# Performance work log

Measured on AMD Instinct MI355X. Metric: run time of the kernel, lower is better.

## Reference

```python
import jax, jax.numpy as jnp
import numpy as np

NE = 256          # number of electrons
D = 256           # attention_dim = num_heads * heads_dim
H = 4             # num_heads
DH = 64           # heads_dim
L = 2             # num_layers
NDETS = 1
MASK_LEN = 0.1


def _ln(x, s, b):
    m = jnp.mean(x, -1, keepdims=True)
    v = jnp.var(x, -1, keepdims=True)
    return (x - m) * jax.lax.rsqrt(v + 1e-5) * s + b


def setup_inputs() -> dict:
    key = jax.random.key(0)
    ks = jax.random.split(key, 16)
    n = lambda k, sh, sc: (jax.random.normal(k, sh) * sc).astype(jnp.float32)
    theta = jax.random.uniform(ks[0], (NE,), minval=0.1, maxval=np.pi - 0.1)
    phi = jax.random.uniform(ks[1], (NE,), minval=0.0, maxval=2.0 * np.pi)
    return {
        "electrons": jnp.stack([theta, phi], -1).astype(jnp.float32),
        "W_in": n(ks[2], (3, D), 3 ** -0.5),
        "Wq": n(ks[3], (L, D, H, DH), D ** -0.5),
        "bq": jnp.zeros((L, H, DH), jnp.float32),
        "Wk": n(ks[4], (L, D, H, DH), D ** -0.5),
        "bk": jnp.zeros((L, H, DH), jnp.float32),
        "Wv": n(ks[5], (L, D, H, DH), D ** -0.5),
        "bv": jnp.zeros((L, H, DH), jnp.float32),
        "Wo": n(ks[6], (L, H, DH, D), D ** -0.5),
        "bo": jnp.zeros((L, D), jnp.float32),
        "W1": n(ks[7], (L, D, D), D ** -0.5),
        "ln1_s": jnp.ones((L, D), jnp.float32),
        "ln1_b": jnp.zeros((L, D), jnp.float32),
        "W2": n(ks[8], (L, D, D), D ** -0.5),
        "b2": jnp.zeros((L, D), jnp.float32),
        "ln2_s": jnp.ones((L, D), jnp.float32),
        "ln2_b": jnp.zeros((L, D), jnp.float32),
        "Worb_r": n(ks[9], (D, NDETS * 2), D ** -0.5),
        "Worb_i": n(ks[10], (D, NDETS * 2), D ** -0.5),
    }


def reference(electrons, W_in, Wq, bq, Wk, bk, Wv, bv, Wo, bo, W1, ln1_s, ln1_b,
              W2, b2, ln2_s, ln2_b, Worb_r, Worb_i):
    theta, phi = electrons[..., 0], electrons[..., 1]
    # ---- pair gather: P = NE*(NE-1)/2 unordered pairs ----
    iu, ju = jnp.triu_indices(NE, k=1)
    th_p = jnp.stack([theta[iu], theta[ju]], -1)   # [P, 2]
    ph_p = jnp.stack([phi[iu], phi[ju]], -1)       # [P, 2]
    # input_feature: (cos t, sin t cos p, sin t sin p)
    feat = jnp.stack([jnp.cos(th_p), jnp.sin(th_p) * jnp.cos(ph_p),
                      jnp.sin(th_p) * jnp.sin(ph_p)], -1)  # [P, 2, 3]
    # ---- batched mini-transformer over all pairs (seq len 2) ----
    h = feat @ W_in  # [P, 2, D]
    for l in range(L):
        q = jnp.einsum('psd,dhk->pshk', h, Wq[l]) + bq[l]
        k = jnp.einsum('psd,dhk->pshk', h, Wk[l]) + bk[l]
        v = jnp.einsum('psd,dhk->pshk', h, Wv[l]) + bv[l]
        logits = jnp.einsum('pshk,pthk->phst', q / np.sqrt(DH), k)
        attn = jax.nn.softmax(logits, axis=-1)
        o = jnp.einsum('phst,pthk->pshk', attn, v)
        mha = jnp.einsum('pshk,hkd->psd', o, Wo[l]) + bo[l]
        h = h + mha @ W1[l]
        h = _ln(h, ln1_s[l], ln1_b[l])
        h = h + jnp.tanh(h @ W2[l] + b2[l])
        h = _ln(h, ln2_s[l], ln2_b[l])
    # ---- pair orbitals: complex dense -> [P, ndets, 2 elec, 2 orb] ----
    orb = (h @ Worb_r + 1j * (h @ Worb_i)).astype(jnp.complex64)  # [P, 2, ndets*2]
    orb = orb.reshape(-1, 2, NDETS, 2).transpose(0, 2, 1, 3)      # [P, ndets, 2, 2]
    # ---- pairwise truncation factor ----
    u = jnp.cos(th_p / 2) * jnp.exp(1j * ph_p / 2)   # [P, 2]
    v_ = jnp.sin(th_p / 2) * jnp.exp(-1j * ph_p / 2)
    chord = jnp.abs(u[:, 0] * v_[:, 1] - u[:, 1] * v_[:, 0])
    trunc = 1.0 - jnp.exp(-(chord / MASK_LEN) ** 2)  # [P]
    orb = orb * trunc[:, None, None, None]
    dets = jnp.linalg.det(orb)          # [P, ndets]
    pair_orbs = jnp.sum(dets, axis=-1)  # [P]
    # ---- scatter into antisymmetric NE x NE matrix ----
    pf = jnp.zeros((NE, NE), jnp.complex64).at[iu, ju].set(pair_orbs)
    pf = pf - pf.T
    # ---- cusp matrix ----
    ue = jnp.cos(theta / 2) * jnp.exp(0.5j * phi)   # [NE]
    ve = jnp.sin(theta / 2) * jnp.exp(-0.5j * phi)
    elem = ue[:, None] * ve[None, :] - ve[:, None] * ue[None, :]  # [NE, NE]
    eye = jnp.eye(NE, dtype=jnp.float32)
    elem_c = elem + eye
    rho_c = jnp.abs(elem_c)
    cusp = elem_c * jnp.exp(-(rho_c / MASK_LEN) ** 2)
    # ---- pfaffian = sqrt(det), in log space for stability ----
    sign, logabs = jnp.linalg.slogdet(pf + cusp)
    log_ferm = 0.5 * (logabs.astype(jnp.complex64) + 1j * jnp.angle(sign))
    # ---- bosonic flux attachment (truncated product), in log space ----
    rho = jnp.abs(elem)
    masked = jnp.sqrt(MASK_LEN ** 2 + rho ** 2) * elem / (rho + eye) + eye
    log_bos = jnp.sum(jnp.log(masked.astype(jnp.complex64)))
    return log_ferm + log_bos
```

## Files before the change

### kernel.cpp

```cpp
#include <hip/hip_runtime.h>
#include <math.h>
#include <stdint.h>

#define NE 256
#define DD 256
#define NL 2
#define P_TOT 32640
#define NB 32
#define NBP 40
#define NPANEL (NE / NB)
#define NXCD 8

typedef __bf16 bf16x8 __attribute__((ext_vector_type(8)));
typedef float f32x4 __attribute__((ext_vector_type(4)));

__device__ __forceinline__ float bf2f(ushort h) {
    union { unsigned u; float f; } c; c.u = ((unsigned)h) << 16; return c.f;
}
__device__ __forceinline__ ushort f2bf(float f) {
    union { float f; unsigned u; } c; c.f = f;
    unsigned u = c.u;
    return (ushort)((u + 0x7fffu + ((u >> 16) & 1u)) >> 16);
}

#define GLD16(gp, lp) __builtin_amdgcn_global_load_lds( \
    (const __attribute__((address_space(1))) unsigned int*)(uintptr_t)(gp), \
    (__attribute__((address_space(3))) unsigned int*)(uintptr_t)(lp), 16, 0, 0)

__global__ void idx_k(int* __restrict__ ip, int* __restrict__ jp) {
    int i = threadIdx.x;
    int base = i * 255 - (i * (i - 1)) / 2;
    for (int j = i + 1; j < NE; ++j) {
        ip[base + j - i - 1] = i;
        jp[base + j - i - 1] = j;
    }
}

__global__ void zero_k(float* __restrict__ acc) {
    if (threadIdx.x < 8) acc[threadIdx.x] = 0.f;
}

__global__ __launch_bounds__(256) void prep_w_k(
    const float* __restrict__ Wq, const float* __restrict__ Wk, const float* __restrict__ Wv,
    const float* __restrict__ Wo, const float* __restrict__ W1, const float* __restrict__ W2,
    ushort* __restrict__ Wqkv_t, ushort* __restrict__ Woth_t) {
    __shared__ float Ts[32][33];
    int z = blockIdx.z, l = z / 6, m = z % 6;
    const float* src;
    ushort* dst;
    if (m == 0)      { src = Wq + l * 65536; dst = Wqkv_t + (size_t)l * 768 * 256 + 0 * 65536; }
    else if (m == 1) { src = Wk + l * 65536; dst = Wqkv_t + (size_t)l * 768 * 256 + 1 * 65536; }
    else if (m == 2) { src = Wv + l * 65536; dst = Wqkv_t + (size_t)l * 768 * 256 + 2 * 65536; }
    else             { src = (m == 3 ? Wo : m == 4 ? W1 : W2) + l * 65536;
                       dst = Woth_t + (size_t)(l * 3 + (m - 3)) * 65536; }
    int k0 = blockIdx.x * 32, n0 = blockIdx.y * 32;
    int t = threadIdx.x, tr = t >> 5, tc = t & 31;
    for (int i = tr; i < 32; i += 8) Ts[i][tc] = src[(size_t)(k0 + i) * 256 + n0 + tc];
    __syncthreads();
    for (int i = tr; i < 32; i += 8) dst[(size_t)(n0 + i) * 256 + k0 + tc] = f2bf(Ts[tc][i]);
}

__global__ void prep_b_k(const float* __restrict__ bq, const float* __restrict__ bk,
                         const float* __restrict__ bv, float* __restrict__ bqkv) {
    int l = blockIdx.x, t = threadIdx.x;
    bqkv[l * 768 + t] = bq[l * 256 + t];
    bqkv[l * 768 + 256 + t] = bk[l * 256 + t];
    bqkv[l * 768 + 512 + t] = bv[l * 256 + t];
}

__global__ __launch_bounds__(256) void fuse_w_k(
    const float* __restrict__ Wo, const float* __restrict__ W1,
    ushort* __restrict__ Wf_t) {
    __shared__ float WoS[32][33];
    __shared__ float W1S[32][33];
    int l = blockIdx.z;
    int n0 = blockIdx.x * 32, d0 = blockIdx.y * 32;
    const float* wo = Wo + l * 65536;
    const float* w1 = W1 + l * 65536;
    int t = threadIdx.x, ty = t >> 5, tx = t & 31;
    float acc4[4] = {0.f, 0.f, 0.f, 0.f};
    for (int m0 = 0; m0 < 256; m0 += 32) {
        __syncthreads();
        for (int i = ty; i < 32; i += 8) {
            WoS[i][tx] = wo[(size_t)(d0 + i) * 256 + m0 + tx];
            W1S[i][tx] = w1[(size_t)(m0 + i) * 256 + n0 + tx];
        }
        __syncthreads();
#pragma unroll
        for (int jm = 0; jm < 32; ++jm) {
            float a = WoS[tx][jm];
#pragma unroll
            for (int q = 0; q < 4; ++q)
                acc4[q] += a * W1S[jm][ty + 8 * q];
        }
    }
#pragma unroll
    for (int q = 0; q < 4; ++q)
        Wf_t[(size_t)l * 65536 + (size_t)(n0 + ty + 8 * q) * 256 + d0 + tx] = f2bf(acc4[q]);
}

__global__ void fuse_b_k(const float* __restrict__ bo, const float* __restrict__ W1,
                         float* __restrict__ bfuse) {
    int l = blockIdx.x, n = threadIdx.x;
    const float* w1 = W1 + l * 65536;
    const float* b = bo + l * 256;
    float s = 0.f;
    for (int m = 0; m < 256; ++m) s += b[m] * w1[(size_t)m * 256 + n];
    bfuse[l * 256 + n] = s;
}

__global__ __launch_bounds__(256) void embed_k(
    const float* __restrict__ el, const float* __restrict__ Win,
    const int* __restrict__ ip, const int* __restrict__ jp,
    ushort* __restrict__ h, int P0) {
    int w = threadIdx.x >> 6, lane = threadIdx.x & 63;
    int r = blockIdx.x * 4 + w;
    int gp = P0 + (r >> 1);
    int e = (r & 1) ? jp[gp] : ip[gp];
    float th = el[2 * e], ph = el[2 * e + 1];
    float st = sinf(th);
    float f0 = cosf(th), f1 = st * cosf(ph), f2 = st * sinf(ph);
    int n = lane * 4;
    float4 w0 = *(const float4*)&Win[n];
    float4 w1 = *(const float4*)&Win[256 + n];
    float4 w2 = *(const float4*)&Win[512 + n];
    ushort4 o;
    o.x = f2bf(f0 * w0.x + f1 * w1.x + f2 * w2.x);
    o.y = f2bf(f0 * w0.y + f1 * w1.y + f2 * w2.y);
    o.z = f2bf(f0 * w0.z + f1 * w1.z + f2 * w2.z);
    o.w = f2bf(f0 * w0.w + f1 * w1.w + f2 * w2.w);
    *(ushort4*)&h[(size_t)r * 256 + n] = o;
}

template <bool BIAS, bool RES>
__global__ __launch_bounds__(256) void gemm_k(
    const ushort* __restrict__ A, int lda,
    const ushort* __restrict__ Bt,
    const float* __restrict__ bias,
    const ushort* __restrict__ Rm, int ldr,
    ushort* __restrict__ C, int ldc, int ny) {
    __shared__ ushort As[128 * 64];
    __shared__ ushort Bs[128 * 64];
    int t = threadIdx.x, lane = t & 63, w = t >> 6;
    int nwg = gridDim.x;
    int orig = blockIdx.x;
    int qq = nwg / NXCD, rr = nwg % NXCD;
    int xcd = orig % NXCD, idx = orig / NXCD;
    int wg = (xcd < rr ? xcd * (qq + 1) : rr * (qq + 1) + (xcd - rr) * qq) + idx;
    int row0 = (wg / ny) * 128, col0 = (wg % ny) * 128;
    int lrow = lane >> 3;
    int kx = ((lane & 7) ^ lrow) << 3;
    const ushort* gA = A + (size_t)(row0 + w * 32 + lrow) * lda + kx;
    const ushort* gB = Bt + (size_t)(col0 + w * 32 + lrow) * 256 + kx;
    f32x4 acc[4][4];
#pragma unroll
    for (int i = 0; i < 4; ++i)
#pragma unroll
        for (int j = 0; j < 4; ++j) acc[i][j] = (f32x4){0.f, 0.f, 0.f, 0.f};
    int wm = w >> 1, wn = w & 1;
    int mbase = wm * 64 + (lane & 15);
    int nbase = wn * 64 + (lane & 15);
    int l7 = lane & 7;
    for (int k0 = 0; k0 < 256; k0 += 64) {
        __syncthreads();
#pragma unroll
        for (int c2 = 0; c2 < 4; ++c2) {
            GLD16(gA + (size_t)(c2 * 8) * lda + k0, &As[(w * 4 + c2) * 512]);
            GLD16(gB + (size_t)(c2 * 8) * 256 + k0, &Bs[(w * 4 + c2) * 512]);
        }
        __syncthreads();
#pragma unroll
        for (int ks = 0; ks < 2; ++ks) {
            int kb = ks * 4 + (lane >> 4);
            bf16x8 af[4], bfr[4];
#pragma unroll
            for (int tm = 0; tm < 4; ++tm)
                af[tm] = *(const bf16x8*)&As[(mbase + tm * 16) * 64 + ((kb ^ l7) << 3)];
#pragma unroll
            for (int tn = 0; tn < 4; ++tn)
                bfr[tn] = *(const bf16x8*)&Bs[(nbase + tn * 16) * 64 + ((kb ^ l7) << 3)];
#pragma unroll
            for (int tm = 0; tm < 4; ++tm)
#pragma unroll
                for (int tn = 0; tn < 4; ++tn)
                    acc[tm][tn] = __builtin_amdgcn_mfma_f32_16x16x32_bf16(
                        af[tm], bfr[tn], acc[tm][tn], 0, 0, 0);
        }
    }
    int q = lane >> 4;
    int crow = row0 + wm * 64 + q * 4;
    int ccol = col0 + wn * 64 + (lane & 15);
#pragma unroll
    for (int tm = 0; tm < 4; ++tm)
#pragma unroll
        for (int r = 0; r < 4; ++r) {
            int row = crow + tm * 16 + r;
#pragma unroll
            for (int tn = 0; tn < 4; ++tn) {
                int col = ccol + tn * 16;
                float v = acc[tm][tn][r];
                if (BIAS) v += bias[col];
                if (RES) v += bf2f(Rm[(size_t)row * ldr + col]);
                C[(size_t)row * ldc + col] = f2bf(v);
            }
        }
}

__global__ __launch_bounds__(256) void attn_k(ushort* __restrict__ qkv) {
    int wid = threadIdx.x >> 6, lane = threadIdx.x & 63;
    int gw = blockIdx.x * 4 + wid;
    int p = gw >> 2, hh = gw & 3;
    size_t r0 = (size_t)(2 * p) * 768 + hh * 64 + lane;
    size_t r1 = r0 + 768;
    float q0 = bf2f(qkv[r0]) * 0.125f, q1 = bf2f(qkv[r1]) * 0.125f;
    float k0 = bf2f(qkv[r0 + 256]), k1 = bf2f(qkv[r1 + 256]);
    float v0 = bf2f(qkv[r0 + 512]), v1 = bf2f(qkv[r1 + 512]);
    float s00 = q0 * k0, s01 = q0 * k1, s10 = q1 * k0, s11 = q1 * k1;
#pragma unroll
    for (int off = 32; off; off >>= 1) {
        s00 += __shfl_xor(s00, off, 64);
        s01 += __shfl_xor(s01, off, 64);
        s10 += __shfl_xor(s10, off, 64);
        s11 += __shfl_xor(s11, off, 64);
    }
    float m0 = fmaxf(s00, s01), m1 = fmaxf(s10, s11);
    float e00 = expf(s00 - m0), e01 = expf(s01 - m0);
    float e10 = expf(s10 - m1), e11 = expf(s11 - m1);
    float i0 = 1.f / (e00 + e01), i1 = 1.f / (e10 + e11);
    float o0 = (e00 * i0) * v0 + (e01 * i0) * v1;
    float o1 = (e10 * i1) * v0 + (e11 * i1) * v1;
    qkv[r0] = f2bf(o0);
    qkv[r1] = f2bf(o1);
}

__global__ __launch_bounds__(256) void ln_a_k(
    const ushort* __restrict__ X, int ldx, ushort* __restrict__ H,
    const float* __restrict__ sc, const float* __restrict__ bi) {
    int w = threadIdx.x >> 6, lane = threadIdx.x & 63;
    int r = blockIdx.x * 4 + w;
    int d0 = lane * 4;
    ushort4 xv = *(const ushort4*)&X[(size_t)r * ldx + d0];
    float x[4] = {bf2f(xv.x), bf2f(xv.y), bf2f(xv.z), bf2f(xv.w)};
    float sum = x[0] + x[1] + x[2] + x[3];
    float sq = x[0] * x[0] + x[1] * x[1] + x[2] * x[2] + x[3] * x[3];
#pragma unroll
    for (int off = 32; off; off >>= 1) {
        sum += __shfl_xor(sum, off, 64);
        sq += __shfl_xor(sq, off, 64);
    }
    float m = sum * (1.f / 256.f);
    float var = sq * (1.f / 256.f) - m * m;
    float rs = rsqrtf(var + 1e-5f);
    float4 s4 = *(const float4*)&sc[d0];
    float4 b4 = *(const float4*)&bi[d0];
    ushort4 o;
    o.x = f2bf((x[0] - m) * rs * s4.x + b4.x);
    o.y = f2bf((x[1] - m) * rs * s4.y + b4.y);
    o.z = f2bf((x[2] - m) * rs * s4.z + b4.z);
    o.w = f2bf((x[3] - m) * rs * s4.w + b4.w);
    *(ushort4*)&H[(size_t)r * 256 + d0] = o;
}

__global__ __launch_bounds__(256) void ln_b_k(
    ushort* __restrict__ H, const ushort* __restrict__ T,
    const float* __restrict__ sc, const float* __restrict__ bi) {
    int w = threadIdx.x >> 6, lane = threadIdx.x & 63;
    int r = blockIdx.x * 4 + w;
    int d0 = lane * 4;
    ushort4 hv = *(const ushort4*)&H[(size_t)r * 256 + d0];
    ushort4 tv = *(const ushort4*)&T[(size_t)r * 256 + d0];
    float x[4];
    x[0] = bf2f(hv.x) + tanhf(bf2f(tv.x));
    x[1] = bf2f(hv.y) + tanhf(bf2f(tv.y));
    x[2] = bf2f(hv.z) + tanhf(bf2f(tv.z));
    x[3] = bf2f(hv.w) + tanhf(bf2f(tv.w));
    float sum = x[0] + x[1] + x[2] + x[3];
    float sq = x[0] * x[0] + x[1] * x[1] + x[2] * x[2] + x[3] * x[3];
#pragma unroll
    for (int off = 32; off; off >>= 1) {
        sum += __shfl_xor(sum, off, 64);
        sq += __shfl_xor(sq, off, 64);
    }
    float m = sum * (1.f / 256.f);
    float var = sq * (1.f / 256.f) - m * m;
    float rs = rsqrtf(var + 1e-5f);
    float4 s4 = *(const float4*)&sc[d0];
    float4 b4 = *(const float4*)&bi[d0];
    ushort4 o;
    o.x = f2bf((x[0] - m) * rs * s4.x + b4.x);
    o.y = f2bf((x[1] - m) * rs * s4.y + b4.y);
    o.z = f2bf((x[2] - m) * rs * s4.z + b4.z);
    o.w = f2bf((x[3] - m) * rs * s4.w + b4.w);
    *(ushort4*)&H[(size_t)r * 256 + d0] = o;
}

__global__ __launch_bounds__(256) void orb_k(
    const ushort* __restrict__ h, const float* __restrict__ Wr, const float* __restrict__ Wi,
    const float* __restrict__ el, const int* __restrict__ ip, const int* __restrict__ jp,
    float2* __restrict__ porb, int P0) {
    int w = threadIdx.x >> 6, lane = threadIdx.x & 63;
    int p = blockIdx.x * 4 + w;
    const ushort* h0 = h + (size_t)(2 * p) * 256;
    int d0 = lane * 4;
    ushort4 a0 = *(const ushort4*)&h0[d0];
    ushort4 a1 = *(const ushort4*)&h0[256 + d0];
    float x0[4] = {bf2f(a0.x), bf2f(a0.y), bf2f(a0.z), bf2f(a0.w)};
    float x1[4] = {bf2f(a1.x), bf2f(a1.y), bf2f(a1.z), bf2f(a1.w)};
    float wrv[8], wiv[8];
    *(float4*)&wrv[0] = *(const float4*)&Wr[2 * d0];
    *(float4*)&wrv[4] = *(const float4*)&Wr[2 * d0 + 4];
    *(float4*)&wiv[0] = *(const float4*)&Wi[2 * d0];
    *(float4*)&wiv[4] = *(const float4*)&Wi[2 * d0 + 4];
    float s[8] = {0, 0, 0, 0, 0, 0, 0, 0};
#pragma unroll
    for (int u = 0; u < 4; ++u) {
        s[0] += x0[u] * wrv[2 * u];     s[1] += x0[u] * wiv[2 * u];
        s[2] += x0[u] * wrv[2 * u + 1]; s[3] += x0[u] * wiv[2 * u + 1];
        s[4] += x1[u] * wrv[2 * u];     s[5] += x1[u] * wiv[2 * u];
        s[6] += x1[u] * wrv[2 * u + 1]; s[7] += x1[u] * wiv[2 * u + 1];
    }
#pragma unroll
    for (int off = 32; off; off >>= 1) {
#pragma unroll
        for (int q2 = 0; q2 < 8; ++q2) s[q2] += __shfl_xor(s[q2], off, 64);
    }
    if (lane == 0) {
        int gp = P0 + p;
        int i = ip[gp], j = jp[gp];
        float thi = el[2 * i], phi_ = el[2 * i + 1];
        float thj = el[2 * j], phj = el[2 * j + 1];
        float chi = cosf(thi * 0.5f), shi = sinf(thi * 0.5f);
        float chj = cosf(thj * 0.5f), shj = sinf(thj * 0.5f);
        float cpi = cosf(phi_ * 0.5f), spi = sinf(phi_ * 0.5f);
        float cpj = cosf(phj * 0.5f), spj = sinf(phj * 0.5f);
        float uix = chi * cpi, uiy = chi * spi;
        float vix = shi * cpi, viy = -shi * spi;
        float ujx = chj * cpj, ujy = chj * spj;
        float vjx = shj * cpj, vjy = -shj * spj;
        float crx = (uix * vjx - uiy * vjy) - (ujx * vix - ujy * viy);
        float cry = (uix * vjy + uiy * vjx) - (ujx * viy + ujy * vix);
        float chord2 = crx * crx + cry * cry;
        float trunc = 1.f - expf(-100.f * chord2);
        float t2 = trunc * trunc;
        float dr = (s[0] * s[6] - s[1] * s[7]) - (s[2] * s[4] - s[3] * s[5]);
        float di = (s[0] * s[7] + s[1] * s[6]) - (s[2] * s[5] + s[3] * s[4]);
        porb[gp] = make_float2(dr * t2, di * t2);
    }
}

__global__ __launch_bounds__(256) void assemble_k(
    const float* __restrict__ el, const float2* __restrict__ porb,
    float2* __restrict__ Am, float* acc) {
    __shared__ float sre[256], sim[256];
    int idx = blockIdx.x * 256 + threadIdx.x;
    int i = idx >> 8, j = idx & 255;
    float thi = el[2 * i], phi_ = el[2 * i + 1];
    float thj = el[2 * j], phj = el[2 * j + 1];
    float chi = cosf(thi * 0.5f), shi = sinf(thi * 0.5f);
    float chj = cosf(thj * 0.5f), shj = sinf(thj * 0.5f);
    float cpi = cosf(phi_ * 0.5f), spi = sinf(phi_ * 0.5f);
    float cpj = cosf(phj * 0.5f), spj = sinf(phj * 0.5f);
    float uix = chi * cpi, uiy = chi * spi;
    float vix = shi * cpi, viy = -shi * spi;
    float ujx = chj * cpj, ujy = chj * spj;
    float vjx = shj * cpj, vjy = -shj * spj;
    float ex = (uix * vjx - uiy * vjy) - (ujx * vix - ujy * viy);
    float ey = (uix * vjy + uiy * vjx) - (ujx * viy + ujy * vix);
    float pfx = 0.f, pfy = 0.f;
    if (i < j) {
        int pp = i * 255 - (i * (i - 1)) / 2 + (j - i - 1);
        float2 t = porb[pp]; pfx = t.x; pfy = t.y;
    } else if (i > j) {
        int pp = j * 255 - (j * (j - 1)) / 2 + (i - j - 1);
        float2 t = porb[pp]; pfx = -t.x; pfy = -t.y;
    }
    float eye = (i == j) ? 1.f : 0.f;
    float ecx = ex + eye, ecy = ey;
    float wgt = expf(-100.f * (ecx * ecx + ecy * ecy));
    Am[idx] = make_float2(pfx + ecx * wgt, pfy + ecy * wgt);
    float lre = 0.f, lim = 0.f;
    if (i != j) {
        float r2 = ex * ex + ey * ey;
        lre = 0.5f * logf(0.01f + r2);
        lim = atan2f(ey, ex);
    }
    sre[threadIdx.x] = lre; sim[threadIdx.x] = lim;
    __syncthreads();
    for (int s2 = 128; s2; s2 >>= 1) {
        if (threadIdx.x < s2) {
            sre[threadIdx.x] += sre[threadIdx.x + s2];
            sim[threadIdx.x] += sim[threadIdx.x + s2];
        }
        __syncthreads();
    }
    if (threadIdx.x == 0) {
        atomicAdd(acc + 0, sre[0]);
        atomicAdd(acc + 1, sim[0]);
    }
}

__device__ __forceinline__ unsigned wave_max_u32_dpp(unsigned m) {
#define DPP_STEP(ctrl) { \
    unsigned tmp_ = (unsigned)__builtin_amdgcn_update_dpp((int)m, (int)m, ctrl, 0xf, 0xf, false); \
    m = (m >= tmp_) ? m : tmp_; }
    DPP_STEP(0x111)
    DPP_STEP(0x112)
    DPP_STEP(0x114)
    DPP_STEP(0x118)
    DPP_STEP(0x142)
    DPP_STEP(0x143)
#undef DPP_STEP
    return (unsigned)__builtin_amdgcn_readlane((int)m, 63);
}

__global__ __launch_bounds__(256) void panel_k(
    float2* __restrict__ Am, int* __restrict__ pivg, float* __restrict__ acc, int k0) {
    __shared__ float2 Pn[NBP][NE];
    __shared__ alignas(16) unsigned rbest4[2][4];
    __shared__ float2 diag_s[NB];
    __shared__ short piv_s[NB];
    int t = threadIdx.x, lane = t & 63, w = t >> 6;
    int nr = NE - k0;
    bool act = t < nr;
    float2 cur = make_float2(0.f, 0.f);
    if (act) {
        const float4* src = (const float4*)(Am + (size_t)(k0 + t) * NE + k0);
#pragma unroll
        for (int c2 = 0; c2 < NB / 2; ++c2) {
            float4 v = src[c2];
            Pn[2 * c2][t]     = make_float2(v.x, v.y);
            Pn[2 * c2 + 1][t] = make_float2(v.z, v.w);
            if (c2 == 0) cur = make_float2(v.x, v.y);
        }
    }
    __syncthreads();
    int lg = t;
    int nsw = 0;
#pragma unroll 1
    for (int j = 0; j < NB; ++j) {
        const int par = j & 1;
        unsigned pk = 0u;
        if (act && lg >= j) {
            float fv = fabsf(cur.x) + fabsf(cur.y);
            union { float f; unsigned u; } cu; cu.f = fv;
            pk = (cu.u & 0xFFFF0000u) | ((unsigned)lg << 8) | (unsigned)t;
        }
        unsigned wbest = wave_max_u32_dpp(pk);
        if (lane == 0) rbest4[par][w] = wbest;
        __syncthreads();
        uint4 rb = *(const uint4*)&rbest4[par][0];
        unsigned ga = rb.x >= rb.y ? rb.x : rb.y;
        unsigned gb = rb.z >= rb.w ? rb.z : rb.w;
        unsigned gg = ga >= gb ? ga : gb;
        int w_phys = (int)(gg & 255u);
        int l_w    = (int)((gg >> 8) & 255u);
        float2 d = Pn[j][w_phys];
        if (t == 0) {
            diag_s[j] = d;
            piv_s[j] = (short)l_w;
            if (l_w != j) nsw++;
        }
        int oldlg = lg;
        if (t == w_phys) lg = j;
        else if (oldlg == j) lg = l_w;
        float ivn = 1.f / (d.x * d.x + d.y * d.y);
        float inx = d.x * ivn, iny = -d.y * ivn;
        if (act && lg > j) {
            float2 L = make_float2(cur.x * inx - cur.y * iny,
                                   cur.x * iny + cur.y * inx);
            Pn[j][t] = L;
            if (j < NB - 1) {
                float2 u1 = Pn[j + 1][w_phys];
                float2 v1 = Pn[j + 1][t];
                v1.x -= L.x * u1.x - L.y * u1.y;
                v1.y -= L.x * u1.y + L.y * u1.x;
                Pn[j + 1][t] = v1;
                cur = v1;
                int nch = (NB - 2 - j + 7) >> 3;
#pragma unroll 1
                for (int ch = 0; ch < nch; ++ch) {
                    int c0 = j + 2 + ch * 8;
                    const float2* ub = &Pn[c0][w_phys];
                    float2* vb = &Pn[c0][t];
                    float2 uu[8], vv[8];
#pragma unroll
                    for (int cc = 0; cc < 8; ++cc) uu[cc] = ub[(size_t)cc * NE];
#pragma unroll
                    for (int cc = 0; cc < 8; ++cc) vv[cc] = vb[(size_t)cc * NE];
#pragma unroll
                    for (int cc = 0; cc < 8; ++cc) {
                        vv[cc].x -= L.x * uu[cc].x - L.y * uu[cc].y;
                        vv[cc].y -= L.x * uu[cc].y + L.y * uu[cc].x;
                    }
#pragma unroll
                    for (int cc = 0; cc < 8; ++cc) vb[(size_t)cc * NE] = vv[cc];
                }
            }
        }
    }
    if (act) {
        float4* dst = (float4*)(Am + (size_t)(k0 + lg) * NE + k0);
#pragma unroll
        for (int c2 = 0; c2 < NB / 2; ++c2) {
            float2 e0 = Pn[2 * c2][t], e1 = Pn[2 * c2 + 1][t];
            dst[c2] = make_float4(e0.x, e0.y, e1.x, e1.y);
        }
    }
    __syncthreads();
    if (t < NB) pivg[t] = k0 + (int)piv_s[t];
    if (w == 0) {
        float lre = 0.f, lim = 0.f;
        if (lane < NB) {
            float2 d = diag_s[lane];
            lre = 0.5f * logf(d.x * d.x + d.y * d.y);
            lim = atan2f(d.y, d.x);
        }
#pragma unroll
        for (int off = 32; off; off >>= 1) {
            lre += __shfl_xor(lre, off, 64);
            lim += __shfl_xor(lim, off, 64);
        }
        if (lane == 0) { acc[2] += lre; acc[3] += lim; }
    }
    if (t == 0) acc[4] += (float)nsw;
}

__global__ __launch_bounds__(256) void trsm_k(
    float2* __restrict__ Am, const int* __restrict__ pivg, int k0) {
    __shared__ float2 Ls[NB][NB + 1];
    __shared__ short sigma[NE];
    __shared__ short rlist[NB];
    __shared__ int rcount;
    int t = threadIdx.x;
    sigma[t] = (short)t;
    for (int idx = t; idx < NB * NB; idx += 256)
        Ls[idx >> 5][idx & 31] = Am[(size_t)(k0 + (idx >> 5)) * NE + k0 + (idx & 31)];
    if (t < NB) rlist[t] = (short)k0;
    __syncthreads();
    if (t == 0) {
        for (int j = 0; j < NB; ++j) {
            int p = pivg[j], r1 = k0 + j;
            short tmp = sigma[r1]; sigma[r1] = sigma[p]; sigma[p] = tmp;
        }
        int cnt = 0;
        for (int r = k0 + NB; r < NE; ++r)
            if (sigma[r] != r) rlist[cnt++] = (short)r;
        rcount = cnt;
    }
    __syncthreads();
    int ncols = NE - k0 - NB;
    if (t >= ncols) return;
    int col = k0 + NB + t;
    int cnt = rcount;
    float2 x[NB];
#pragma unroll
    for (int i = 0; i < NB; ++i)
        x[i] = Am[(size_t)sigma[k0 + i] * NE + col];
    float2 extra[NB];
#pragma unroll
    for (int q = 0; q < NB; ++q)
        extra[q] = Am[(size_t)sigma[rlist[q]] * NE + col];
#pragma unroll
    for (int i = 1; i < NB; ++i) {
        float2 xi = x[i];
#pragma unroll
        for (int j = 0; j < i; ++j) {
            float2 l = Ls[i][j];
            xi.x -= l.x * x[j].x - l.y * x[j].y;
            xi.y -= l.x * x[j].y + l.y * x[j].x;
        }
        x[i] = xi;
    }
#pragma unroll
    for (int i = 0; i < NB; ++i)
        Am[(size_t)(k0 + i) * NE + col] = x[i];
#pragma unroll
    for (int q = 0; q < NB; ++q)
        if (q < cnt) Am[(size_t)rlist[q] * NE + col] = extra[q];
}

__global__ __launch_bounds__(256) void update_k(float2* __restrict__ Am, int k0) {
    __shared__ float2 Lt[NB][NB + 1];
    __shared__ float2 Ut[NB][NB + 1];
    int t = threadIdx.x;
    int r0 = k0 + NB + blockIdx.x * NB;
    int c0 = k0 + NB + blockIdx.y * NB;
    for (int idx = t; idx < NB * NB; idx += 256) {
        int a = idx >> 5, b = idx & 31;
        Lt[a][b] = Am[(size_t)(r0 + a) * NE + k0 + b];
        Ut[a][b] = Am[(size_t)(k0 + a) * NE + c0 + b];
    }
    __syncthreads();
    int lr = t >> 3, lc0 = (t & 7) * 4;
    float2 s0 = {0.f, 0.f}, s1 = {0.f, 0.f}, s2 = {0.f, 0.f}, s3 = {0.f, 0.f};
#pragma unroll
    for (int k = 0; k < NB; ++k) {
        float2 a = Lt[lr][k];
        float2 u0 = Ut[k][lc0 + 0], u1 = Ut[k][lc0 + 1];
        float2 u2 = Ut[k][lc0 + 2], u3 = Ut[k][lc0 + 3];
        s0.x += a.x * u0.x - a.y * u0.y; s0.y += a.x * u0.y + a.y * u0.x;
        s1.x += a.x * u1.x - a.y * u1.y; s1.y += a.x * u1.y + a.y * u1.x;
        s2.x += a.x * u2.x - a.y * u2.y; s2.y += a.x * u2.y + a.y * u2.x;
        s3.x += a.x * u3.x - a.y * u3.y; s3.y += a.x * u3.y + a.y * u3.x;
    }
    size_t base = (size_t)(r0 + lr) * NE + c0 + lc0;
    float2 cc;
    cc = Am[base + 0]; cc.x -= s0.x; cc.y -= s0.y; Am[base + 0] = cc;
    cc = Am[base + 1]; cc.x -= s1.x; cc.y -= s1.y; Am[base + 1] = cc;
    cc = Am[base + 2]; cc.x -= s2.x; cc.y -= s2.y; Am[base + 2] = cc;
    cc = Am[base + 3]; cc.x -= s3.x; cc.y -= s3.y; Am[base + 3] = cc;
}

__global__ void finalize_k(const float* __restrict__ acc, float* __restrict__ out) {
    if (threadIdx.x == 0) {
        float ang = acc[3] + 3.14159265358979323846f * acc[4];
        ang -= 6.283185307179586f * rintf(ang * 0.15915494309189535f);
        out[0] = 0.5f * acc[2] + acc[0];
        out[1] = 0.5f * ang + acc[1];
    }
}

extern "C" void kernel_launch(void* const* d_in, const int* in_sizes, int n_in,
                              void* d_out, int out_size, void* d_ws, size_t ws_size,
                              hipStream_t stream) {
    (void)in_sizes; (void)n_in; (void)out_size;
    const float* el   = (const float*)d_in[0];
    const float* Win  = (const float*)d_in[1];
    const float* Wq   = (const float*)d_in[2];
    const float* bq   = (const float*)d_in[3];
    const float* Wk   = (const float*)d_in[4];
    const float* bk   = (const float*)d_in[5];
    const float* Wv   = (const float*)d_in[6];
    const float* bv   = (const float*)d_in[7];
    const float* Wo   = (const float*)d_in[8];
    const float* bo   = (const float*)d_in[9];
    const float* W1   = (const float*)d_in[10];
    const float* ln1s = (const float*)d_in[11];
    const float* ln1b = (const float*)d_in[12];
    const float* W2   = (const float*)d_in[13];
    const float* b2   = (const float*)d_in[14];
    const float* ln2s = (const float*)d_in[15];
    const float* ln2b = (const float*)d_in[16];
    const float* Wor  = (const float*)d_in[17];
    const float* Woi  = (const float*)d_in[18];

    char* wp = (char*)d_ws;
    auto alloc = [&](size_t b) {
        char* r = wp;
        wp += (b + 255) & ~(size_t)255;
        return r;
    };
    int*    ipb  = (int*)alloc((size_t)P_TOT * 4);
    int*    jpb  = (int*)alloc((size_t)P_TOT * 4);
    float2* porb = (float2*)alloc((size_t)P_TOT * 8);
    float2* Am   = (float2*)alloc((size_t)NE * NE * 8);
    float*  acc  = (float*)alloc(256);
    int*    pivg = (int*)alloc((size_t)NE * 4);
    ushort* Wqkv_t = (ushort*)alloc((size_t)2 * 768 * 256 * 2);
    ushort* Woth_t = (ushort*)alloc((size_t)6 * 65536 * 2);
    ushort* Wf_t   = (ushort*)alloc((size_t)2 * 65536 * 2);
    float*  bfuse  = (float*)alloc((size_t)2 * 256 * 4);
    float*  bqkv = (float*)alloc((size_t)2 * 768 * 4);
    size_t fixed = (size_t)(wp - (char*)d_ws);

    int nchunk = 0, PCr = 0, MCr = 0;
    const int cands[3] = {1, 2, 3};
    for (int ci = 0; ci < 3; ++ci) {
        int pc = P_TOT / cands[ci];
        size_t mc = (size_t)2 * pc;
        size_t var = 0;
        var += ((mc * 256 * 2 + 255) & ~(size_t)255);
        var += ((mc * 768 * 2 + 255) & ~(size_t)255);
        var += ((mc * 256 * 2 + 255) & ~(size_t)255);
        if (fixed + var <= ws_size) { nchunk = cands[ci]; PCr = pc; MCr = (int)mc; break; }
    }
    if (!nchunk) {
        zero_k<<<1, 64, 0, stream>>>((float*)d_out);
        return;
    }
    ushort* hb   = (ushort*)alloc((size_t)MCr * 256 * 2);
    ushort* qkvb = (ushort*)alloc((size_t)MCr * 768 * 2);
    ushort* tb   = (ushort*)alloc((size_t)MCr * 256 * 2);
    int MTr = MCr / 128;

    prep_w_k<<<dim3(8, 8, 12), 256, 0, stream>>>(Wq, Wk, Wv, Wo, W1, W2, Wqkv_t, Woth_t);
    prep_b_k<<<2, 256, 0, stream>>>(bq, bk, bv, bqkv);
    fuse_w_k<<<dim3(8, 8, 2), 256, 0, stream>>>(Wo, W1, Wf_t);
    fuse_b_k<<<2, 256, 0, stream>>>(bo, W1, bfuse);
    idx_k<<<1, 256, 0, stream>>>(ipb, jpb);
    zero_k<<<1, 64, 0, stream>>>(acc);

    for (int c = 0; c < nchunk; ++c) {
        int P0 = c * PCr;
        embed_k<<<MCr / 4, 256, 0, stream>>>(el, Win, ipb, jpb, hb, P0);
        for (int l = 0; l < NL; ++l) {
            gemm_k<true, false><<<MTr * 6, 256, 0, stream>>>(
                hb, 256, Wqkv_t + (size_t)l * 768 * 256, bqkv + l * 768, nullptr, 0, qkvb, 768, 6);
            attn_k<<<PCr, 256, 0, stream>>>(qkvb);
            gemm_k<true, true><<<MTr * 2, 256, 0, stream>>>(
                qkvb, 768, Wf_t + (size_t)l * 65536, bfuse + l * 256, hb, 256, tb, 256, 2);
            ln_a_k<<<MCr / 4, 256, 0, stream>>>(tb, 256, hb, ln1s + l * 256, ln1b + l * 256);
            gemm_k<true, false><<<MTr * 2, 256, 0, stream>>>(
                hb, 256, Woth_t + (size_t)(l * 3 + 2) * 65536, b2 + l * 256, nullptr, 0, tb, 256, 2);
            ln_b_k<<<MCr / 4, 256, 0, stream>>>(hb, tb, ln2s + l * 256, ln2b + l * 256);
        }
        orb_k<<<PCr / 4, 256, 0, stream>>>(hb, Wor, Woi, el, ipb, jpb, porb, P0);
    }
    assemble_k<<<NE, 256, 0, stream>>>(el, porb, Am, acc);

    for (int p = 0; p < NPANEL; ++p) {
        int k0 = p * NB;
        panel_k<<<1, 256, 0, stream>>>(Am, pivg + p * NB, acc, k0);
        int m = NE - k0 - NB;
        if (m > 0) {
            trsm_k<<<1, 256, 0, stream>>>(Am, pivg + p * NB, k0);
            dim3 ug(m / NB, m / NB);
            update_k<<<ug, 256, 0, stream>>>(Am, k0);
        }
    }
    finalize_k<<<1, 64, 0, stream>>>(acc, (float*)d_out);
}
```

Baseline: 974.2 us.

## Fuse layernorms into full-row GEMM epilogues and merge TRSM into panel kernel

Adds a GEMM kernel whose block covers a full 256-column row tile, so the bias, residual, optional tanh and layernorm are applied in the epilogue and written back in place. This removes the separate layernorm kernels, the temporary buffer tb and its round trips through memory. The triangular solve is also folded into the panel kernel, reading L from shared memory instead of global, which saves seven launches in the serial LU chain. In exchange, each GEMM launches a quarter as many blocks, each holding more accumulator registers and shared memory, which may lower occupancy and parallelism.

```diff
diff --git a/kernel.cpp b/kernel.cpp
--- a/kernel.cpp
+++ b/kernel.cpp
@@ -206,6 +206,109 @@
         }
 }
 
+template <bool TANH>
+__global__ __launch_bounds__(256) void gemm_ln_k(
+    const ushort* __restrict__ A, int lda,
+    const ushort* __restrict__ Bt,
+    const float* __restrict__ bias,
+    const ushort* __restrict__ Rm,
+    const float* __restrict__ sc, const float* __restrict__ bi,
+    ushort* __restrict__ C) {
+    __shared__ ushort As[128 * 64];
+    __shared__ ushort Bs[256 * 64];
+    __shared__ float red_s[128][2][2];
+    int t = threadIdx.x, lane = t & 63, w = t >> 6;
+    int row0 = blockIdx.x * 128;
+    int lrow = lane >> 3;
+    int kx = ((lane & 7) ^ lrow) << 3;
+    const ushort* gA = A + (size_t)(row0 + w * 32 + lrow) * lda + kx;
+    const ushort* gB = Bt + (size_t)(w * 64 + lrow) * 256 + kx;
+    f32x4 acc[4][8];
+#pragma unroll
+    for (int i = 0; i < 4; ++i)
+#pragma unroll
+        for (int j = 0; j < 8; ++j) acc[i][j] = (f32x4){0.f, 0.f, 0.f, 0.f};
+    int wm = w >> 1, wn = w & 1;
+    int mbase = wm * 64 + (lane & 15);
+    int nbase = wn * 128 + (lane & 15);
+    int l7 = lane & 7;
+    for (int k0 = 0; k0 < 256; k0 += 64) {
+        __syncthreads();
+#pragma unroll
+        for (int c2 = 0; c2 < 4; ++c2)
+            GLD16(gA + (size_t)(c2 * 8) * lda + k0, &As[(w * 4 + c2) * 512]);
+#pragma unroll
+        for (int c2 = 0; c2 < 8; ++c2)
+            GLD16(gB + (size_t)(c2 * 8) * 256 + k0, &Bs[(w * 8 + c2) * 512]);
+        __syncthreads();
+#pragma unroll
+        for (int ks = 0; ks < 2; ++ks) {
+            int kb = ks * 4 + (lane >> 4);
+            bf16x8 af[4], bfr[8];
+#pragma unroll
+            for (int tm = 0; tm < 4; ++tm)
+                af[tm] = *(const bf16x8*)&As[(mbase + tm * 16) * 64 + ((kb ^ l7) << 3)];
+#pragma unroll
+            for (int tn = 0; tn < 8; ++tn)
+                bfr[tn] = *(const bf16x8*)&Bs[(nbase + tn * 16) * 64 + ((kb ^ l7) << 3)];
+#pragma unroll
+            for (int tm = 0; tm < 4; ++tm)
+#pragma unroll
+                for (int tn = 0; tn < 8; ++tn)
+                    acc[tm][tn] = __builtin_amdgcn_mfma_f32_16x16x32_bf16(
+                        af[tm], bfr[tn], acc[tm][tn], 0, 0, 0);
+        }
+    }
+    int q = lane >> 4;
+#pragma unroll
+    for (int tm = 0; tm < 4; ++tm)
+#pragma unroll
+        for (int r = 0; r < 4; ++r) {
+            int rl = wm * 64 + tm * 16 + q * 4 + r;
+            int row = row0 + rl;
+            float s = 0.f, sq = 0.f;
+#pragma unroll
+            for (int tn = 0; tn < 8; ++tn) {
+                int col = wn * 128 + (lane & 15) + tn * 16;
+                float v = acc[tm][tn][r] + bias[col];
+                float x;
+                if (TANH) x = bf2f(Rm[(size_t)row * 256 + col]) + tanhf(v);
+                else      x = v + bf2f(Rm[(size_t)row * 256 + col]);
+                acc[tm][tn][r] = x;
+                s += x; sq += x * x;
+            }
+#pragma unroll
+            for (int off = 1; off <= 8; off <<= 1) {
+                s += __shfl_xor(s, off, 64);
+                sq += __shfl_xor(sq, off, 64);
+            }
+            if ((lane & 15) == 0) { red_s[rl][wn][0] = s; red_s[rl][wn][1] = sq; }
+        }
+    __syncthreads();
+    float sc8[8], bi8[8];
+#pragma unroll
+    for (int tn = 0; tn < 8; ++tn) {
+        int col = wn * 128 + (lane & 15) + tn * 16;
+        sc8[tn] = sc[col]; bi8[tn] = bi[col];
+    }
+#pragma unroll
+    for (int tm = 0; tm < 4; ++tm)
+#pragma unroll
+        for (int r = 0; r < 4; ++r) {
+            int rl = wm * 64 + tm * 16 + q * 4 + r;
+            int row = row0 + rl;
+            float m = (red_s[rl][0][0] + red_s[rl][1][0]) * (1.f / 256.f);
+            float var = (red_s[rl][0][1] + red_s[rl][1][1]) * (1.f / 256.f) - m * m;
+            float rs = rsqrtf(var + 1e-5f);
+#pragma unroll
+            for (int tn = 0; tn < 8; ++tn) {
+                int col = wn * 128 + (lane & 15) + tn * 16;
+                C[(size_t)row * 256 + col] =
+                    f2bf((acc[tm][tn][r] - m) * rs * sc8[tn] + bi8[tn]);
+            }
+        }
+}
+
 __global__ __launch_bounds__(256) void attn_k(ushort* __restrict__ qkv) {
     int wid = threadIdx.x >> 6, lane = threadIdx.x & 63;
     int gw = blockIdx.x * 4 + wid;
@@ -231,67 +334,6 @@
     float o1 = (e10 * i1) * v0 + (e11 * i1) * v1;
     qkv[r0] = f2bf(o0);
     qkv[r1] = f2bf(o1);
-}
-
-__global__ __launch_bounds__(256) void ln_a_k(
-    const ushort* __restrict__ X, int ldx, ushort* __restrict__ H,
-    const float* __restrict__ sc, const float* __restrict__ bi) {
-    int w = threadIdx.x >> 6, lane = threadIdx.x & 63;
-    int r = blockIdx.x * 4 + w;
-    int d0 = lane * 4;
-    ushort4 xv = *(const ushort4*)&X[(size_t)r * ldx + d0];
-    float x[4] = {bf2f(xv.x), bf2f(xv.y), bf2f(xv.z), bf2f(xv.w)};
-    float sum = x[0] + x[1] + x[2] + x[3];
-    float sq = x[0] * x[0] + x[1] * x[1] + x[2] * x[2] + x[3] * x[3];
-#pragma unroll
-    for (int off = 32; off; off >>= 1) {
-        sum += __shfl_xor(sum, off, 64);
-        sq += __shfl_xor(sq, off, 64);
-    }
-    float m = sum * (1.f / 256.f);
-    float var = sq * (1.f / 256.f) - m * m;
-    float rs = rsqrtf(var + 1e-5f);
-    float4 s4 = *(const float4*)&sc[d0];
-    float4 b4 = *(const float4*)&bi[d0];
-    ushort4 o;
-    o.x = f2bf((x[0] - m) * rs * s4.x + b4.x);
-    o.y = f2bf((x[1] - m) * rs * s4.y + b4.y);
-    o.z = f2bf((x[2] - m) * rs * s4.z + b4.z);
-    o.w = f2bf((x[3] - m) * rs * s4.w + b4.w);
-    *(ushort4*)&H[(size_t)r * 256 + d0] = o;
-}
-
-__global__ __launch_bounds__(256) void ln_b_k(
-    ushort* __restrict__ H, const ushort* __restrict__ T,
-    const float* __restrict__ sc, const float* __restrict__ bi) {
-    int w = threadIdx.x >> 6, lane = threadIdx.x & 63;
-    int r = blockIdx.x * 4 + w;
-    int d0 = lane * 4;
-    ushort4 hv = *(const ushort4*)&H[(size_t)r * 256 + d0];
-    ushort4 tv = *(const ushort4*)&T[(size_t)r * 256 + d0];
-    float x[4];
-    x[0] = bf2f(hv.x) + tanhf(bf2f(tv.x));
-    x[1] = bf2f(hv.y) + tanhf(bf2f(tv.y));
-    x[2] = bf2f(hv.z) + tanhf(bf2f(tv.z));
-    x[3] = bf2f(hv.w) + tanhf(bf2f(tv.w));
-    float sum = x[0] + x[1] + x[2] + x[3];
-    float sq = x[0] * x[0] + x[1] * x[1] + x[2] * x[2] + x[3] * x[3];
-#pragma unroll
-    for (int off = 32; off; off >>= 1) {
-        sum += __shfl_xor(sum, off, 64);
-        sq += __shfl_xor(sq, off, 64);
-    }
-    float m = sum * (1.f / 256.f);
-    float var = sq * (1.f / 256.f) - m * m;
-    float rs = rsqrtf(var + 1e-5f);
-    float4 s4 = *(const float4*)&sc[d0];
-    float4 b4 = *(const float4*)&bi[d0];
-    ushort4 o;
-    o.x = f2bf((x[0] - m) * rs * s4.x + b4.x);
-    o.y = f2bf((x[1] - m) * rs * s4.y + b4.y);
-    o.z = f2bf((x[2] - m) * rs * s4.z + b4.z);
-    o.w = f2bf((x[3] - m) * rs * s4.w + b4.w);
-    *(ushort4*)&H[(size_t)r * 256 + d0] = o;
 }
 
 __global__ __launch_bounds__(256) void orb_k(
@@ -414,11 +456,16 @@
 }
 
 __global__ __launch_bounds__(256) void panel_k(
-    float2* __restrict__ Am, int* __restrict__ pivg, float* __restrict__ acc, int k0) {
+    float2* __restrict__ Am, float* __restrict__ acc, int k0) {
     __shared__ float2 Pn[NBP][NE];
     __shared__ alignas(16) unsigned rbest4[2][4];
     __shared__ float2 diag_s[NB];
     __shared__ short piv_s[NB];
+    __shared__ short phys_of_s[NB];
+    __shared__ float2 Ls[NB][NB + 1];
+    __shared__ short sigma_s[NE];
+    __shared__ short rlist_s[NB];
+    __shared__ int rcount_s;
     int t = threadIdx.x, lane = t & 63, w = t >> 6;
     int nr = NE - k0;
     bool act = t < nr;
@@ -498,6 +545,7 @@
             }
         }
     }
+    if (act && lg < NB) phys_of_s[lg] = (short)t;
     if (act) {
         float4* dst = (float4*)(Am + (size_t)(k0 + lg) * NE + k0);
 #pragma unroll
@@ -507,7 +555,6 @@
         }
     }
     __syncthreads();
-    if (t < NB) pivg[t] = k0 + (int)piv_s[t];
     if (w == 0) {
         float lre = 0.f, lim = 0.f;
         if (lane < NB) {
@@ -523,51 +570,45 @@
         if (lane == 0) { acc[2] += lre; acc[3] += lim; }
     }
     if (t == 0) acc[4] += (float)nsw;
-}
-
-__global__ __launch_bounds__(256) void trsm_k(
-    float2* __restrict__ Am, const int* __restrict__ pivg, int k0) {
-    __shared__ float2 Ls[NB][NB + 1];
-    __shared__ short sigma[NE];
-    __shared__ short rlist[NB];
-    __shared__ int rcount;
-    int t = threadIdx.x;
-    sigma[t] = (short)t;
-    for (int idx = t; idx < NB * NB; idx += 256)
-        Ls[idx >> 5][idx & 31] = Am[(size_t)(k0 + (idx >> 5)) * NE + k0 + (idx & 31)];
-    if (t < NB) rlist[t] = (short)k0;
+    if (k0 + NB >= NE) return;
+    for (int idx = t; idx < NB * NB; idx += 256) {
+        int i2 = idx >> 5, j2 = idx & 31;
+        Ls[i2][j2] = Pn[j2][phys_of_s[i2]];
+    }
+    sigma_s[t] = (short)t;
+    if (t < NB) rlist_s[t] = (short)k0;
     __syncthreads();
     if (t == 0) {
-        for (int j = 0; j < NB; ++j) {
-            int p = pivg[j], r1 = k0 + j;
-            short tmp = sigma[r1]; sigma[r1] = sigma[p]; sigma[p] = tmp;
+        for (int j2 = 0; j2 < NB; ++j2) {
+            int p = k0 + (int)piv_s[j2], r1 = k0 + j2;
+            short tmp = sigma_s[r1]; sigma_s[r1] = sigma_s[p]; sigma_s[p] = tmp;
         }
         int cnt = 0;
-        for (int r = k0 + NB; r < NE; ++r)
-            if (sigma[r] != r) rlist[cnt++] = (short)r;
-        rcount = cnt;
+        for (int r2 = k0 + NB; r2 < NE; ++r2)
+            if (sigma_s[r2] != r2) rlist_s[cnt++] = (short)r2;
+        rcount_s = cnt;
     }
     __syncthreads();
     int ncols = NE - k0 - NB;
     if (t >= ncols) return;
     int col = k0 + NB + t;
-    int cnt = rcount;
+    int cnt = rcount_s;
     float2 x[NB];
 #pragma unroll
     for (int i = 0; i < NB; ++i)
-        x[i] = Am[(size_t)sigma[k0 + i] * NE + col];
+        x[i] = Am[(size_t)sigma_s[k0 + i] * NE + col];
     float2 extra[NB];
 #pragma unroll
-    for (int q = 0; q < NB; ++q)
-        extra[q] = Am[(size_t)sigma[rlist[q]] * NE + col];
+    for (int q2 = 0; q2 < NB; ++q2)
+        extra[q2] = Am[(size_t)sigma_s[rlist_s[q2]] * NE + col];
 #pragma unroll
     for (int i = 1; i < NB; ++i) {
         float2 xi = x[i];
 #pragma unroll
-        for (int j = 0; j < i; ++j) {
-            float2 l = Ls[i][j];
-            xi.x -= l.x * x[j].x - l.y * x[j].y;
-            xi.y -= l.x * x[j].y + l.y * x[j].x;
+        for (int j2 = 0; j2 < i; ++j2) {
+            float2 l = Ls[i][j2];
+            xi.x -= l.x * x[j2].x - l.y * x[j2].y;
+            xi.y -= l.x * x[j2].y + l.y * x[j2].x;
         }
         x[i] = xi;
     }
@@ -575,8 +616,8 @@
     for (int i = 0; i < NB; ++i)
         Am[(size_t)(k0 + i) * NE + col] = x[i];
 #pragma unroll
-    for (int q = 0; q < NB; ++q)
-        if (q < cnt) Am[(size_t)rlist[q] * NE + col] = extra[q];
+    for (int q2 = 0; q2 < NB; ++q2)
+        if (q2 < cnt) Am[(size_t)rlist_s[q2] * NE + col] = extra[q2];
 }
 
 __global__ __launch_bounds__(256) void update_k(float2* __restrict__ Am, int k0) {
@@ -655,7 +696,6 @@
     float2* porb = (float2*)alloc((size_t)P_TOT * 8);
     float2* Am   = (float2*)alloc((size_t)NE * NE * 8);
     float*  acc  = (float*)alloc(256);
-    int*    pivg = (int*)alloc((size_t)NE * 4);
     ushort* Wqkv_t = (ushort*)alloc((size_t)2 * 768 * 256 * 2);
     ushort* Woth_t = (ushort*)alloc((size_t)6 * 65536 * 2);
     ushort* Wf_t   = (ushort*)alloc((size_t)2 * 65536 * 2);
@@ -671,7 +711,6 @@
         size_t var = 0;
         var += ((mc * 256 * 2 + 255) & ~(size_t)255);
         var += ((mc * 768 * 2 + 255) & ~(size_t)255);
-        var += ((mc * 256 * 2 + 255) & ~(size_t)255);
         if (fixed + var <= ws_size) { nchunk = cands[ci]; PCr = pc; MCr = (int)mc; break; }
     }
     if (!nchunk) {
@@ -680,7 +719,6 @@
     }
     ushort* hb   = (ushort*)alloc((size_t)MCr * 256 * 2);
     ushort* qkvb = (ushort*)alloc((size_t)MCr * 768 * 2);
-    ushort* tb   = (ushort*)alloc((size_t)MCr * 256 * 2);
     int MTr = MCr / 128;
 
     prep_w_k<<<dim3(8, 8, 12), 256, 0, stream>>>(Wq, Wk, Wv, Wo, W1, W2, Wqkv_t, Woth_t);
@@ -697,12 +735,12 @@
             gemm_k<true, false><<<MTr * 6, 256, 0, stream>>>(
                 hb, 256, Wqkv_t + (size_t)l * 768 * 256, bqkv + l * 768, nullptr, 0, qkvb, 768, 6);
             attn_k<<<PCr, 256, 0, stream>>>(qkvb);
-            gemm_k<true, true><<<MTr * 2, 256, 0, stream>>>(
-                qkvb, 768, Wf_t + (size_t)l * 65536, bfuse + l * 256, hb, 256, tb, 256, 2);
-            ln_a_k<<<MCr / 4, 256, 0, stream>>>(tb, 256, hb, ln1s + l * 256, ln1b + l * 256);
-            gemm_k<true, false><<<MTr * 2, 256, 0, stream>>>(
-                hb, 256, Woth_t + (size_t)(l * 3 + 2) * 65536, b2 + l * 256, nullptr, 0, tb, 256, 2);
-            ln_b_k<<<MCr / 4, 256, 0, stream>>>(hb, tb, ln2s + l * 256, ln2b + l * 256);
+            gemm_ln_k<false><<<MTr, 256, 0, stream>>>(
+                qkvb, 768, Wf_t + (size_t)l * 65536, bfuse + l * 256, hb,
+                ln1s + l * 256, ln1b + l * 256, hb);
+            gemm_ln_k<true><<<MTr, 256, 0, stream>>>(
+                hb, 256, Woth_t + (size_t)(l * 3 + 2) * 65536, b2 + l * 256, hb,
+                ln2s + l * 256, ln2b + l * 256, hb);
         }
         orb_k<<<PCr / 4, 256, 0, stream>>>(hb, Wor, Woi, el, ipb, jpb, porb, P0);
     }
@@ -710,10 +748,9 @@
 
     for (int p = 0; p < NPANEL; ++p) {
         int k0 = p * NB;
-        panel_k<<<1, 256, 0, stream>>>(Am, pivg + p * NB, acc, k0);
+        panel_k<<<1, 256, 0, stream>>>(Am, acc, k0);
         int m = NE - k0 - NB;
         if (m > 0) {
-            trsm_k<<<1, 256, 0, stream>>>(Am, pivg + p * NB, k0);
             dim3 ug(m / NB, m / NB);
             update_k<<<ug, 256, 0, stream>>>(Am, k0);
         }
```

New measurement: 1.003 ms. 2.9% more time.
